# Performance work log

Measured on AMD Instinct MI355X. Metric: run time of the kernel, lower is better.

The kernel has to match this reference:

```python
import jax, jax.numpy as jnp
import numpy as np

HIDDEN = 256
HEADS = 8
HEAD_DIM = HIDDEN // HEADS
N = 4096
EPS = 1e-5


def setup_inputs() -> dict:
    key = jax.random.key(0)
    ks = jax.random.split(key, 16)
    s = HIDDEN ** -0.5
    inp = {
        "A": jax.random.uniform(ks[0], (N, N), dtype=jnp.float32),
        "h": jax.random.normal(ks[1], (N, HIDDEN), dtype=jnp.float32),
        # Linear layers stored torch-style as [out, in]
        "Wq": jax.random.normal(ks[2], (HIDDEN, HIDDEN), jnp.float32) * s,
        "bq": jnp.zeros((HIDDEN,), jnp.float32),
        "Wk": jax.random.normal(ks[3], (HIDDEN, HIDDEN), jnp.float32) * s,
        "bk": jnp.zeros((HIDDEN,), jnp.float32),
        "Wv": jax.random.normal(ks[4], (HIDDEN, HIDDEN), jnp.float32) * s,
        "bv": jnp.zeros((HIDDEN,), jnp.float32),
        "Wo": jax.random.normal(ks[5], (HIDDEN, HIDDEN), jnp.float32) * s,
        "bo": jnp.zeros((HIDDEN,), jnp.float32),
        "W1": jax.random.normal(ks[6], (2 * HIDDEN, HIDDEN), jnp.float32) * s,
        "c1": jnp.zeros((2 * HIDDEN,), jnp.float32),
        "W2": jax.random.normal(ks[7], (HIDDEN, 2 * HIDDEN), jnp.float32) * (2 * HIDDEN) ** -0.5,
        "c2": jnp.zeros((HIDDEN,), jnp.float32),
        "g1": jnp.ones((HIDDEN,), jnp.float32),
        "be1": jnp.zeros((HIDDEN,), jnp.float32),
        "g2": jnp.ones((HIDDEN,), jnp.float32),
        "be2": jnp.zeros((HIDDEN,), jnp.float32),
    }
    return inp


def _batchnorm(x, gamma, beta):
    # BatchNorm1d training mode: biased batch stats over node axis
    mean = x.mean(axis=0)
    var = ((x - mean) ** 2).mean(axis=0)
    return (x - mean) * jax.lax.rsqrt(var + EPS) * gamma + beta


def _mha(A, h, Wq, bq, Wk, bk, Wv, bv, Wo, bo):
    n = h.shape[0]
    scaling = HEAD_DIM ** -0.5
    # NOTE: raw reshape [N, H*d] -> (H, N, d), exactly as the torch code (no transpose)
    q = ((h @ Wq.T + bq).reshape(HEADS, n, HEAD_DIM)) * scaling
    k = (h @ Wk.T + bk).reshape(HEADS, n, HEAD_DIM)
    v = (h @ Wv.T + bv).reshape(HEADS, n, HEAD_DIM)
    t = jnp.einsum('hnd,hmd->hnm', q, k)          # [H, N, N]
    attn = jax.nn.softmax(t * A, axis=2)          # multiplicative adjacency mask
    out = jnp.einsum('hnm,hmd->hnd', attn, v)     # [H, N, d]
    return out.reshape(n, -1) @ Wo.T + bo         # raw reshape back, as in torch


def reference(A, h, Wq, bq, Wk, bk, Wv, bv, Wo, bo, W1, c1, W2, c2, g1, be1, g2, be2):
    h1 = h
    x = _mha(A, h, Wq, bq, Wk, bk, Wv, bv, Wo, bo)
    x = _batchnorm(x + h1, g1, be1)
    h2 = x
    x = jax.nn.relu(x @ W1.T + c1) @ W2.T + c2
    return _batchnorm(h2 + x, g2, be2)
```

## Files before the change

### kernel.cpp

```cpp
#include <hip/hip_runtime.h>

#define N_NODES 4096
#define HID 256
#define NHEADS 8
#define HDIM 32
#define EPSV 1e-5f
#define M2LOG 11.541560327111707f

typedef __bf16 bf16x8 __attribute__((ext_vector_type(8)));
typedef __bf16 bf16x4 __attribute__((ext_vector_type(4)));
typedef float f32x4 __attribute__((ext_vector_type(4)));

__device__ inline float fexp2(float x) {
    float r;
    asm("v_exp_f32 %0, %1" : "=v"(r) : "v"(x));
    return r;
}

__device__ inline uint4 pack8(float4 a, float4 b) {
    bf16x8 p;
    p[0]=(__bf16)a.x; p[1]=(__bf16)a.y; p[2]=(__bf16)a.z; p[3]=(__bf16)a.w;
    p[4]=(__bf16)b.x; p[5]=(__bf16)b.y; p[6]=(__bf16)b.z; p[7]=(__bf16)b.w;
    return __builtin_bit_cast(uint4, p);
}
__device__ inline float4 nmad4(float4 x, float4 s, float4 sh) {
    return make_float4(fmaf(x.x,s.x,sh.x), fmaf(x.y,s.y,sh.y),
                       fmaf(x.z,s.z,sh.z), fmaf(x.w,s.w,sh.w));
}
__device__ inline float bflo(unsigned u) { return __builtin_bit_cast(float, u << 16); }
__device__ inline float bfhi(unsigned u) { return __builtin_bit_cast(float, u & 0xFFFF0000u); }

__launch_bounds__(256)
__global__ void gemm_mfma(const float* __restrict__ X, const float* __restrict__ W,
                          const float* __restrict__ bias, const float* __restrict__ resid,
                          float* __restrict__ C,
                          const float* __restrict__ pSin, const float* __restrict__ pQin,
                          const float* __restrict__ gamin, const float* __restrict__ betin,
                          int norm_x, int norm_r,
                          float* __restrict__ psum, float* __restrict__ pq,
                          int M, int N, int K, float scale, int do_relu) {
    __shared__ uint4 xl[2][512];
    __shared__ uint4 wl[2][256];
    __shared__ __align__(16) float nsc[256];
    __shared__ __align__(16) float nsh[256];
    const int bm = blockIdx.x * 64, bn = blockIdx.y * 32;
    const int t = threadIdx.x;
    const int w = t >> 6, l = t & 63, g = l >> 4, nl = l & 15;
    const int srow = t >> 3, seg = t & 7;
    const int sx = (seg & 3) << 1;
    const int d0 = seg*64 + (srow ^ sx);
    const int d1 = seg*64 + ((srow + 32) ^ sx);
    const int dw = seg*32 + (srow ^ sx);
    const float* xp = X + (size_t)(bm + srow)*K + seg*8;
    const float* wp = W + (size_t)(bn + srow)*K + seg*8;
    const size_t rstep = (size_t)32*K;

    if (pSin) {
        float s = 0.f, q = 0.f;
        #pragma unroll 8
        for (int b = 0; b < 64; ++b) { s += pSin[b*HID + t]; q += pQin[b*HID + t]; }
        const float m = s * (1.f/4096.f);
        const float rstd = rsqrtf(q*(1.f/4096.f) - m*m + EPSV);
        const float sc = rstd * gamin[t];
        nsc[t] = sc;
        nsh[t] = fmaf(-m, sc, betin[t]);
        __syncthreads();
    }

    f32x4 acc[2];
    acc[0] = (f32x4){0.f,0.f,0.f,0.f};
    acc[1] = (f32x4){0.f,0.f,0.f,0.f};

    {
        float4 x0 = *(const float4*)(xp),          x1 = *(const float4*)(xp + 4);
        float4 x2 = *(const float4*)(xp + rstep),  x3 = *(const float4*)(xp + rstep + 4);
        if (norm_x) {
            float4 s0 = *(const float4*)(nsc + seg*8), s1 = *(const float4*)(nsc + seg*8 + 4);
            float4 h0 = *(const float4*)(nsh + seg*8), h1 = *(const float4*)(nsh + seg*8 + 4);
            x0 = nmad4(x0,s0,h0); x1 = nmad4(x1,s1,h1);
            x2 = nmad4(x2,s0,h0); x3 = nmad4(x3,s1,h1);
        }
        float4 w0 = *(const float4*)(wp), w1 = *(const float4*)(wp + 4);
        xl[0][d0] = pack8(x0, x1); xl[0][d1] = pack8(x2, x3);
        wl[0][dw] = pack8(w0, w1);
    }
    __syncthreads();

    for (int k0 = 0; k0 < K; k0 += 64) {
        const int cur = (k0 >> 6) & 1;
        const bool nxt = (k0 + 64) < K;
        float4 nx0, nx1, nx2, nx3, nw0, nw1;
        if (nxt) {
            const int kk = k0 + 64;
            nx0 = *(const float4*)(xp + kk);          nx1 = *(const float4*)(xp + kk + 4);
            nx2 = *(const float4*)(xp + rstep + kk);  nx3 = *(const float4*)(xp + rstep + kk + 4);
            if (norm_x) {
                float4 s0 = *(const float4*)(nsc + kk + seg*8), s1 = *(const float4*)(nsc + kk + seg*8 + 4);
                float4 h0 = *(const float4*)(nsh + kk + seg*8), h1 = *(const float4*)(nsh + kk + seg*8 + 4);
                nx0 = nmad4(nx0,s0,h0); nx1 = nmad4(nx1,s1,h1);
                nx2 = nmad4(nx2,s0,h0); nx3 = nmad4(nx3,s1,h1);
            }
            nw0 = *(const float4*)(wp + kk);  nw1 = *(const float4*)(wp + kk + 4);
        }
        __builtin_amdgcn_s_setprio(1);
        #pragma unroll
        for (int ks = 0; ks < 2; ++ks) {
            bf16x8 af = __builtin_bit_cast(bf16x8, xl[cur][(ks*4 + g)*64 + ((w*16 + nl) ^ (g << 1))]);
            #pragma unroll
            for (int nf = 0; nf < 2; ++nf) {
                bf16x8 bfr = __builtin_bit_cast(bf16x8, wl[cur][(ks*4 + g)*32 + ((nf*16 + nl) ^ (g << 1))]);
                acc[nf] = __builtin_amdgcn_mfma_f32_16x16x32_bf16(af, bfr, acc[nf], 0, 0, 0);
            }
        }
        __builtin_amdgcn_s_setprio(0);
        if (nxt) {
            xl[cur^1][d0] = pack8(nx0, nx1); xl[cur^1][d1] = pack8(nx2, nx3);
            wl[cur^1][dw] = pack8(nw0, nw1);
        }
        __syncthreads();
    }

    float colS[2] = {0.f,0.f}, colQ[2] = {0.f,0.f};
    #pragma unroll
    for (int nf = 0; nf < 2; ++nf) {
        const int col = bn + nf*16 + nl;
        const float bb = bias[col];
        float rs = 1.f, rh = 0.f;
        if (norm_r) { rs = nsc[col]; rh = nsh[col]; }
        #pragma unroll
        for (int r = 0; r < 4; ++r) {
            const int row = bm + w*16 + g*4 + r;
            float v = acc[nf][r] + bb;
            if (resid) {
                float rv = resid[(size_t)row*N + col];
                v += norm_r ? fmaf(rv, rs, rh) : rv;
            }
            v *= scale;
            if (do_relu) v = fmaxf(v, 0.f);
            C[(size_t)row*N + col] = v;
            colS[nf] += v;
            colQ[nf] = fmaf(v, v, colQ[nf]);
        }
    }
    if (psum) {
        float* cs = (float*)&xl[0][0];
        float* cq = cs + 512;
        #pragma unroll
        for (int nf = 0; nf < 2; ++nf) {
            const int idx = (w*4 + g)*32 + nf*16 + nl;
            cs[idx] = colS[nf];
            cq[idx] = colQ[nf];
        }
        __syncthreads();
        if (t < 32) {
            float s = 0.f, q = 0.f;
            #pragma unroll
            for (int i = 0; i < 16; ++i) { s += cs[i*32 + t]; q += cq[i*32 + t]; }
            psum[blockIdx.x*HID + bn + t] = s;
            pq[blockIdx.x*HID + bn + t]   = q;
        }
    }
}

__launch_bounds__(256)
__global__ void gemm_wo(const __bf16* __restrict__ Opart, const float* __restrict__ Lpart,
                        int nsplit, const float* __restrict__ W,
                        const float* __restrict__ bias, const float* __restrict__ resid,
                        float* __restrict__ C, float* __restrict__ psum, float* __restrict__ pq) {
    const int N = 256, K = 256;
    __shared__ uint4 xl[2][512];
    __shared__ uint4 wl[2][256];
    const int bm = blockIdx.x * 64, bn = blockIdx.y * 32;
    const int t = threadIdx.x;
    const int w = t >> 6, l = t & 63, g = l >> 4, nl = l & 15;
    const int srow = t >> 3, seg = t & 7;
    const int sx = (seg & 3) << 1;
    const int d0 = seg*64 + (srow ^ sx);
    const int d1 = seg*64 + ((srow + 32) ^ sx);
    const int dw = seg*32 + (srow ^ sx);
    const float* wrow = W + (size_t)(bn + srow)*K;

    auto cl = [&](int row, int kp, float4& a, float4& b) {
        const size_t flat = (size_t)row*256 + kp;
        const int hn = (int)(flat >> 5);
        float L = 0.f;
        float s0=0,s1=0,s2=0,s3=0,s4=0,s5=0,s6=0,s7=0;
        for (int z = 0; z < nsplit; ++z) {
            L += Lpart[z*32768 + hn];
            uint4 u = *(const uint4*)(Opart + (size_t)z*1048576 + flat);
            s0 += bflo(u.x); s1 += bfhi(u.x);
            s2 += bflo(u.y); s3 += bfhi(u.y);
            s4 += bflo(u.z); s5 += bfhi(u.z);
            s6 += bflo(u.w); s7 += bfhi(u.w);
        }
        const float inv = 1.f / L;
        a = make_float4(s0*inv, s1*inv, s2*inv, s3*inv);
        b = make_float4(s4*inv, s5*inv, s6*inv, s7*inv);
    };
    auto wld = [&](int kp, float4& a, float4& b) {
        const int kb = (kp & ~31) + ((kp >> 3) & 3)*4;
        a = *(const float4*)(wrow + kb);
        b = *(const float4*)(wrow + kb + 16);
    };

    f32x4 acc[2];
    acc[0] = (f32x4){0.f,0.f,0.f,0.f};
    acc[1] = (f32x4){0.f,0.f,0.f,0.f};

    {
        float4 x0, x1, x2, x3, w0, w1;
        cl(bm + srow,      seg*8, x0, x1);
        cl(bm + srow + 32, seg*8, x2, x3);
        wld(seg*8, w0, w1);
        xl[0][d0] = pack8(x0, x1); xl[0][d1] = pack8(x2, x3);
        wl[0][dw] = pack8(w0, w1);
    }
    __syncthreads();

    for (int k0 = 0; k0 < K; k0 += 64) {
        const int cur = (k0 >> 6) & 1;
        const bool nxt = (k0 + 64) < K;
        float4 nx0, nx1, nx2, nx3, nw0, nw1;
        if (nxt) {
            const int kp = k0 + 64 + seg*8;
            cl(bm + srow,      kp, nx0, nx1);
            cl(bm + srow + 32, kp, nx2, nx3);
            wld(kp, nw0, nw1);
        }
        __builtin_amdgcn_s_setprio(1);
        #pragma unroll
        for (int ks = 0; ks < 2; ++ks) {
            bf16x8 af = __builtin_bit_cast(bf16x8, xl[cur][(ks*4 + g)*64 + ((w*16 + nl) ^ (g << 1))]);
            #pragma unroll
            for (int nf = 0; nf < 2; ++nf) {
                bf16x8 bfr = __builtin_bit_cast(bf16x8, wl[cur][(ks*4 + g)*32 + ((nf*16 + nl) ^ (g << 1))]);
                acc[nf] = __builtin_amdgcn_mfma_f32_16x16x32_bf16(af, bfr, acc[nf], 0, 0, 0);
            }
        }
        __builtin_amdgcn_s_setprio(0);
        if (nxt) {
            xl[cur^1][d0] = pack8(nx0, nx1); xl[cur^1][d1] = pack8(nx2, nx3);
            wl[cur^1][dw] = pack8(nw0, nw1);
        }
        __syncthreads();
    }

    float colS[2] = {0.f,0.f}, colQ[2] = {0.f,0.f};
    #pragma unroll
    for (int nf = 0; nf < 2; ++nf) {
        const int col = bn + nf*16 + nl;
        const float bb = bias[col];
        #pragma unroll
        for (int r = 0; r < 4; ++r) {
            const int row = bm + w*16 + g*4 + r;
            float v = acc[nf][r] + bb + resid[(size_t)row*N + col];
            C[(size_t)row*N + col] = v;
            colS[nf] += v;
            colQ[nf] = fmaf(v, v, colQ[nf]);
        }
    }
    {
        float* cs = (float*)&xl[0][0];
        float* cq = cs + 512;
        #pragma unroll
        for (int nf = 0; nf < 2; ++nf) {
            const int idx = (w*4 + g)*32 + nf*16 + nl;
            cs[idx] = colS[nf];
            cq[idx] = colQ[nf];
        }
        __syncthreads();
        if (t < 32) {
            float s = 0.f, q = 0.f;
            #pragma unroll
            for (int i = 0; i < 16; ++i) { s += cs[i*32 + t]; q += cq[i*32 + t]; }
            psum[blockIdx.x*HID + bn + t] = s;
            pq[blockIdx.x*HID + bn + t]   = q;
        }
    }
}

__launch_bounds__(256)
__global__ void gemm_qkv3(const float* __restrict__ X,
                          const float* __restrict__ Wq, const float* __restrict__ Wk,
                          const float* __restrict__ Wv, const float* __restrict__ bq,
                          const float* __restrict__ bk, const float* __restrict__ bv,
                          __bf16* __restrict__ qhat, __bf16* __restrict__ khat,
                          __bf16* __restrict__ vT) {
    const int K = 256;
    __shared__ uint4 xl[2][512];
    __shared__ uint4 wql[2][256];
    __shared__ uint4 wkl[2][256];
    __shared__ uint4 wvl[2][256];
    const int bm = blockIdx.x * 64, bn = blockIdx.y * 32;
    const int t = threadIdx.x;
    const int w = t >> 6, l = t & 63, g = l >> 4, nl = l & 15;
    const int srow = t >> 3, seg = t & 7;
    const int sx = (seg & 3) << 1;
    const int d0 = seg*64 + (srow ^ sx);
    const int d1 = seg*64 + ((srow + 32) ^ sx);
    const int dw = seg*32 + (srow ^ sx);
    const float* xp  = X  + (size_t)(bm + srow)*K + seg*8;
    const float* wqp = Wq + (size_t)(bn + srow)*K + seg*8;
    const float* wkp = Wk + (size_t)(bn + srow)*K + seg*8;
    const float* wvp = Wv + (size_t)(bn + srow)*K + seg*8;
    const size_t rstep = (size_t)32*K;

    f32x4 aq[2], ak[2], av[2];
    #pragma unroll
    for (int nf = 0; nf < 2; ++nf) {
        aq[nf] = (f32x4){0.f,0.f,0.f,0.f};
        ak[nf] = (f32x4){0.f,0.f,0.f,0.f};
        av[nf] = (f32x4){0.f,0.f,0.f,0.f};
    }

    {
        float4 x0 = *(const float4*)(xp),          x1 = *(const float4*)(xp + 4);
        float4 x2 = *(const float4*)(xp + rstep),  x3 = *(const float4*)(xp + rstep + 4);
        float4 q0 = *(const float4*)(wqp), q1 = *(const float4*)(wqp + 4);
        float4 k0 = *(const float4*)(wkp), k1 = *(const float4*)(wkp + 4);
        float4 v0 = *(const float4*)(wvp), v1 = *(const float4*)(wvp + 4);
        xl[0][d0] = pack8(x0, x1); xl[0][d1] = pack8(x2, x3);
        wql[0][dw] = pack8(q0, q1);
        wkl[0][dw] = pack8(k0, k1);
        wvl[0][dw] = pack8(v0, v1);
    }
    __syncthreads();

    for (int k0 = 0; k0 < K; k0 += 64) {
        const int cur = (k0 >> 6) & 1;
        const bool nxt = (k0 + 64) < K;
        float4 nx0, nx1, nx2, nx3, nq0, nq1, nk0, nk1, nv0, nv1;
        if (nxt) {
            const int kk = k0 + 64;
            nx0 = *(const float4*)(xp + kk);          nx1 = *(const float4*)(xp + kk + 4);
            nx2 = *(const float4*)(xp + rstep + kk);  nx3 = *(const float4*)(xp + rstep + kk + 4);
            nq0 = *(const float4*)(wqp + kk);  nq1 = *(const float4*)(wqp + kk + 4);
            nk0 = *(const float4*)(wkp + kk);  nk1 = *(const float4*)(wkp + kk + 4);
            nv0 = *(const float4*)(wvp + kk);  nv1 = *(const float4*)(wvp + kk + 4);
        }
        __builtin_amdgcn_s_setprio(1);
        #pragma unroll
        for (int ks = 0; ks < 2; ++ks) {
            bf16x8 af = __builtin_bit_cast(bf16x8, xl[cur][(ks*4 + g)*64 + ((w*16 + nl) ^ (g << 1))]);
            #pragma unroll
            for (int nf = 0; nf < 2; ++nf) {
                const int wi = (ks*4 + g)*32 + ((nf*16 + nl) ^ (g << 1));
                bf16x8 bq8 = __builtin_bit_cast(bf16x8, wql[cur][wi]);
                bf16x8 bk8 = __builtin_bit_cast(bf16x8, wkl[cur][wi]);
                bf16x8 bv8 = __builtin_bit_cast(bf16x8, wvl[cur][wi]);
                aq[nf] = __builtin_amdgcn_mfma_f32_16x16x32_bf16(af, bq8, aq[nf], 0, 0, 0);
                ak[nf] = __builtin_amdgcn_mfma_f32_16x16x32_bf16(af, bk8, ak[nf], 0, 0, 0);
                av[nf] = __builtin_amdgcn_mfma_f32_16x16x32_bf16(af, bv8, av[nf], 0, 0, 0);
            }
        }
        __builtin_amdgcn_s_setprio(0);
        if (nxt) {
            xl[cur^1][d0] = pack8(nx0, nx1); xl[cur^1][d1] = pack8(nx2, nx3);
            wql[cur^1][dw] = pack8(nq0, nq1);
            wkl[cur^1][dw] = pack8(nk0, nk1);
            wvl[cur^1][dw] = pack8(nv0, nv1);
        }
        __syncthreads();
    }

    const float qscale = 0.25506595325f;
    #pragma unroll
    for (int nf = 0; nf < 2; ++nf) {
        const int col = bn + nf*16 + nl;
        const float bbq = bq[col], bbk = bk[col], bbv = bv[col];
        const int dd = col & 31;
        #pragma unroll
        for (int r = 0; r < 4; ++r) {
            const int row = bm + w*16 + g*4 + r;
            const int hh = row >> 9;
            const int nn = ((row & 511) << 3) | (col >> 5);
            qhat[((size_t)(hh*4096 + nn))*32 + dd] = (__bf16)((aq[nf][r] + bbq) * qscale);
            khat[((size_t)(hh*4096 + nn))*32 + dd] = (__bf16)(ak[nf][r] + bbk);
            vT[((size_t)(hh*32 + dd))*4096 + nn]   = (__bf16)(av[nf][r] + bbv);
        }
    }
}

__launch_bounds__(512, 2)
__global__ void attn_mfma(const __bf16* __restrict__ qh_, const __bf16* __restrict__ kh,
                          const __bf16* __restrict__ vT, const float* __restrict__ A,
                          __bf16* __restrict__ Opart, float* __restrict__ Lpart, int mlen) {
    __shared__ float A_lds[2][64][68];
    __shared__ uint4 p_lds[8][4][64];

    const int t = threadIdx.x;
    const int w = t >> 6, l = t & 63;
    const int g = l >> 4, nl = l & 15;
    const int n0 = blockIdx.x * 64;
    const int z = blockIdx.y;
    const int m_begin = z * mlen;
    const int nsteps = mlen >> 6;

    bf16x8 qf[4];
    #pragma unroll
    for (int nf = 0; nf < 4; ++nf)
        qf[nf] = *(const bf16x8*)(qh_ + ((size_t)(w*4096 + n0 + nf*16 + nl))*32 + g*8);

    f32x4 oacc[4][2];
    #pragma unroll
    for (int nf = 0; nf < 4; ++nf) {
        oacc[nf][0] = (f32x4){0.f,0.f,0.f,0.f};
        oacc[nf][1] = (f32x4){0.f,0.f,0.f,0.f};
    }
    float Li[4] = {0.f, 0.f, 0.f, 0.f};

    const int aq = t >> 3, am = (t & 7) * 8;
    const float* Abase = A + (size_t)(n0 + aq)*N_NODES + m_begin + am;
    const __bf16* kbase = kh + ((size_t)w*4096 + nl)*32 + g*8;
    const __bf16* vbase = vT + ((size_t)w*32 + nl)*4096 + g*8;

    *(float4*)&A_lds[0][aq][am]   = *(const float4*)(Abase);
    *(float4*)&A_lds[0][aq][am+4] = *(const float4*)(Abase + 4);
    __syncthreads();

    for (int s = 0; s < nsteps; ++s) {
        const int cur = s & 1;
        const int m0 = m_begin + s*64;
        const bool nxt = (s + 1) < nsteps;
        float4 a0n, a1n;
        if (nxt) {
            a0n = *(const float4*)(Abase + (s+1)*64);
            a1n = *(const float4*)(Abase + (s+1)*64 + 4);
        }
        bf16x8 kf[4], vf[4];
        #pragma unroll
        for (int tt = 0; tt < 4; ++tt)
            kf[tt] = *(const bf16x8*)(kbase + (size_t)(m0 + tt*16)*32);
        #pragma unroll
        for (int half = 0; half < 2; ++half)
            #pragma unroll
            for (int dt = 0; dt < 2; ++dt)
                vf[half*2+dt] = *(const bf16x8*)(vbase + (size_t)dt*16*4096 + m0 + half*32);
        __builtin_amdgcn_sched_barrier(0);

        #pragma unroll
        for (int half = 0; half < 2; ++half) {
            #pragma unroll
            for (int tt2 = 0; tt2 < 2; ++tt2) {
                const int tt = half*2 + tt2;
                f32x4 st[4];
                __builtin_amdgcn_s_setprio(1);
                #pragma unroll
                for (int nf = 0; nf < 4; ++nf) {
                    f32x4 zz = (f32x4){0.f,0.f,0.f,0.f};
                    st[nf] = __builtin_amdgcn_mfma_f32_16x16x32_bf16(kf[tt], qf[nf], zz, 0, 0, 0);
                }
                __builtin_amdgcn_s_setprio(0);
                #pragma unroll
                for (int nf = 0; nf < 4; ++nf) {
                    const f32x4 a4 = *(const f32x4*)&A_lds[cur][nf*16 + nl][tt*16 + g*4];
                    float p0 = fexp2(fmaf(st[nf][0], a4[0], -M2LOG));
                    float p1 = fexp2(fmaf(st[nf][1], a4[1], -M2LOG));
                    float p2 = fexp2(fmaf(st[nf][2], a4[2], -M2LOG));
                    float p3 = fexp2(fmaf(st[nf][3], a4[3], -M2LOG));
                    Li[nf] += (p0 + p1) + (p2 + p3);
                    bf16x4 pk;
                    pk[0] = (__bf16)p0; pk[1] = (__bf16)p1;
                    pk[2] = (__bf16)p2; pk[3] = (__bf16)p3;
                    const int gm = tt2*2 + (g >> 1);
                    *(bf16x4*)((char*)&p_lds[w][nf][0] + (gm*16 + (nl ^ (gm << 1)))*16 + (g & 1)*8) = pk;
                }
            }
            __builtin_amdgcn_s_setprio(1);
            #pragma unroll
            for (int nf = 0; nf < 4; ++nf) {
                bf16x8 pf = __builtin_bit_cast(bf16x8, p_lds[w][nf][g*16 + (nl ^ (g << 1))]);
                oacc[nf][0] = __builtin_amdgcn_mfma_f32_16x16x32_bf16(vf[half*2+0], pf, oacc[nf][0], 0, 0, 0);
                oacc[nf][1] = __builtin_amdgcn_mfma_f32_16x16x32_bf16(vf[half*2+1], pf, oacc[nf][1], 0, 0, 0);
            }
            __builtin_amdgcn_s_setprio(0);
        }

        if (nxt) {
            *(float4*)&A_lds[cur^1][aq][am]   = a0n;
            *(float4*)&A_lds[cur^1][aq][am+4] = a1n;
        }
        __syncthreads();
    }

    #pragma unroll
    for (int nf = 0; nf < 4; ++nf) {
        Li[nf] += __shfl_xor(Li[nf], 16);
        Li[nf] += __shfl_xor(Li[nf], 32);
        const int nq = n0 + nf*16 + nl;
        __bf16* ob = Opart + ((size_t)(z*NHEADS + w)*4096 + nq)*32;
        bf16x8 pk8;
        #pragma unroll
        for (int j = 0; j < 4; ++j) {
            pk8[j]     = (__bf16)oacc[nf][0][j];
            pk8[4 + j] = (__bf16)oacc[nf][1][j];
        }
        *(bf16x8*)(ob + g*8) = pk8;
        if (g == 0)
            Lpart[(z*NHEADS + w)*4096 + nq] = Li[nf];
    }
}

__launch_bounds__(256)
__global__ void bnorm_fin_apply(const float* __restrict__ X,
                                const float* __restrict__ pS, const float* __restrict__ pQ,
                                const float* __restrict__ gam, const float* __restrict__ bet,
                                float* __restrict__ Y) {
    __shared__ __align__(16) float sc[256];
    __shared__ __align__(16) float sh[256];
    const int t = threadIdx.x;
    {
        float s = 0.f, q = 0.f;
        #pragma unroll 8
        for (int b = 0; b < 64; ++b) { s += pS[b*HID + t]; q += pQ[b*HID + t]; }
        const float m = s * (1.f/4096.f);
        const float rstd = rsqrtf(q*(1.f/4096.f) - m*m + EPSV);
        const float scv = rstd * gam[t];
        sc[t] = scv;
        sh[t] = fmaf(-m, scv, bet[t]);
    }
    __syncthreads();
    const int base0 = (blockIdx.x * 256 + t) * 16;
    #pragma unroll
    for (int j = 0; j < 4; ++j) {
        const int base = base0 + j*4;
        const int c = base & (HID - 1);
        float4 x = *(const float4*)(X + base);
        float4 o;
        o.x = fmaf(x.x, sc[c+0], sh[c+0]);
        o.y = fmaf(x.y, sc[c+1], sh[c+1]);
        o.z = fmaf(x.z, sc[c+2], sh[c+2]);
        o.w = fmaf(x.w, sc[c+3], sh[c+3]);
        *(float4*)(Y + base) = o;
    }
}

extern "C" void kernel_launch(void* const* d_in, const int* in_sizes, int n_in,
                              void* d_out, int out_size, void* d_ws, size_t ws_size,
                              hipStream_t stream) {
    const float* A  = (const float*)d_in[0];
    const float* h  = (const float*)d_in[1];
    const float* Wq = (const float*)d_in[2];
    const float* bq = (const float*)d_in[3];
    const float* Wk = (const float*)d_in[4];
    const float* bk = (const float*)d_in[5];
    const float* Wv = (const float*)d_in[6];
    const float* bv = (const float*)d_in[7];
    const float* Wo = (const float*)d_in[8];
    const float* bo = (const float*)d_in[9];
    const float* W1 = (const float*)d_in[10];
    const float* c1 = (const float*)d_in[11];
    const float* W2 = (const float*)d_in[12];
    const float* c2 = (const float*)d_in[13];
    const float* g1 = (const float*)d_in[14];
    const float* be1= (const float*)d_in[15];
    const float* g2 = (const float*)d_in[16];
    const float* be2= (const float*)d_in[17];

    char* wsb = (char*)d_ws;
    const size_t MiB = (size_t)1 << 20;
    const int nsplit = (ws_size >= 26*MiB) ? 8 : (ws_size >= 18*MiB) ? 4 : 2;
    const int mlen = N_NODES / nsplit;

    __bf16* qhat = (__bf16*)(wsb + 0*MiB);
    __bf16* khat = (__bf16*)(wsb + 2*MiB);
    __bf16* vT   = (__bf16*)(wsb + 4*MiB);
    __bf16* Opart = (__bf16*)(wsb + 8*MiB);
    float* Lpart = (float*)(wsb + 8*MiB + (size_t)nsplit*2*MiB);
    char* statb  = wsb + 8*MiB + (size_t)nsplit*2*MiB + 1*MiB;
    float* partS1 = (float*)statb;
    float* partQ1 = partS1 + 64*HID;
    float* partS2 = partQ1 + 64*HID;
    float* partQ2 = partS2 + 64*HID;
    float* Y1 = (float*)(wsb + 4*MiB);
    float* F1 = (float*)(wsb + 8*MiB);
    float* Y2 = (float*)(wsb + 0*MiB);

    gemm_qkv3<<<dim3(64, 8), 256, 0, stream>>>(h, Wq, Wk, Wv, bq, bk, bv, qhat, khat, vT);

    attn_mfma<<<dim3(64, nsplit), 512, 0, stream>>>(qhat, khat, vT, A, Opart, Lpart, mlen);

    gemm_wo<<<dim3(64, 8), 256, 0, stream>>>(Opart, Lpart, nsplit, Wo, bo, h, Y1, partS1, partQ1);

    gemm_mfma<<<dim3(64, 16), 256, 0, stream>>>(Y1, W1, c1, nullptr, F1,
                                                partS1, partQ1, g1, be1, 1, 0,
                                                nullptr, nullptr, 4096, 512, 256, 1.f, 1);
    gemm_mfma<<<dim3(64, 8), 256, 0, stream>>>(F1, W2, c2, Y1, Y2,
                                               partS1, partQ1, g1, be1, 0, 1,
                                               partS2, partQ2, 4096, 256, 512, 1.f, 0);

    bnorm_fin_apply<<<256, 256, 0, stream>>>(Y2, partS2, partQ2, g2, be2, (float*)d_out);
}
```

Baseline: 123.4 us.

## Prefetch adjacency tiles two steps ahead and use lightweight LDS barriers

Deepens the prefetch of the adjacency tile A from one step to two, holding two register sets in rotation, so global load latency is covered by two iterations of attention work. The loop is manually unrolled by two with a macro to alternate the register buffers. __syncthreads is replaced by an explicit lgkmcnt wait plus s_barrier, so the barrier does not also wait for outstanding global loads. This raises register pressure and assumes nsteps is even, since the unrolled loop runs step s+1 without checking it.

Measured after the change: 124.5 us. About the same (+0.9%).

```diff
diff --git a/kernel.cpp b/kernel.cpp
--- a/kernel.cpp
+++ b/kernel.cpp
@@ -416,72 +416,86 @@
 
     *(float4*)&A_lds[0][aq][am]   = *(const float4*)(Abase);
     *(float4*)&A_lds[0][aq][am+4] = *(const float4*)(Abase + 4);
-    __syncthreads();
-
-    for (int s = 0; s < nsteps; ++s) {
-        const int cur = s & 1;
-        const int m0 = m_begin + s*64;
-        const bool nxt = (s + 1) < nsteps;
-        float4 a0n, a1n;
-        if (nxt) {
-            a0n = *(const float4*)(Abase + (s+1)*64);
-            a1n = *(const float4*)(Abase + (s+1)*64 + 4);
-        }
-        bf16x8 kf[4], vf[4];
-        #pragma unroll
-        for (int tt = 0; tt < 4; ++tt)
-            kf[tt] = *(const bf16x8*)(kbase + (size_t)(m0 + tt*16)*32);
-        #pragma unroll
-        for (int half = 0; half < 2; ++half)
-            #pragma unroll
-            for (int dt = 0; dt < 2; ++dt)
-                vf[half*2+dt] = *(const bf16x8*)(vbase + (size_t)dt*16*4096 + m0 + half*32);
-        __builtin_amdgcn_sched_barrier(0);
-
-        #pragma unroll
-        for (int half = 0; half < 2; ++half) {
-            #pragma unroll
-            for (int tt2 = 0; tt2 < 2; ++tt2) {
-                const int tt = half*2 + tt2;
-                f32x4 st[4];
-                __builtin_amdgcn_s_setprio(1);
-                #pragma unroll
-                for (int nf = 0; nf < 4; ++nf) {
-                    f32x4 zz = (f32x4){0.f,0.f,0.f,0.f};
-                    st[nf] = __builtin_amdgcn_mfma_f32_16x16x32_bf16(kf[tt], qf[nf], zz, 0, 0, 0);
-                }
-                __builtin_amdgcn_s_setprio(0);
-                #pragma unroll
-                for (int nf = 0; nf < 4; ++nf) {
-                    const f32x4 a4 = *(const f32x4*)&A_lds[cur][nf*16 + nl][tt*16 + g*4];
-                    float p0 = fexp2(fmaf(st[nf][0], a4[0], -M2LOG));
-                    float p1 = fexp2(fmaf(st[nf][1], a4[1], -M2LOG));
-                    float p2 = fexp2(fmaf(st[nf][2], a4[2], -M2LOG));
-                    float p3 = fexp2(fmaf(st[nf][3], a4[3], -M2LOG));
-                    Li[nf] += (p0 + p1) + (p2 + p3);
-                    bf16x4 pk;
-                    pk[0] = (__bf16)p0; pk[1] = (__bf16)p1;
-                    pk[2] = (__bf16)p2; pk[3] = (__bf16)p3;
-                    const int gm = tt2*2 + (g >> 1);
-                    *(bf16x4*)((char*)&p_lds[w][nf][0] + (gm*16 + (nl ^ (gm << 1)))*16 + (g & 1)*8) = pk;
-                }
-            }
-            __builtin_amdgcn_s_setprio(1);
-            #pragma unroll
-            for (int nf = 0; nf < 4; ++nf) {
-                bf16x8 pf = __builtin_bit_cast(bf16x8, p_lds[w][nf][g*16 + (nl ^ (g << 1))]);
-                oacc[nf][0] = __builtin_amdgcn_mfma_f32_16x16x32_bf16(vf[half*2+0], pf, oacc[nf][0], 0, 0, 0);
-                oacc[nf][1] = __builtin_amdgcn_mfma_f32_16x16x32_bf16(vf[half*2+1], pf, oacc[nf][1], 0, 0, 0);
-            }
-            __builtin_amdgcn_s_setprio(0);
-        }
-
-        if (nxt) {
-            *(float4*)&A_lds[cur^1][aq][am]   = a0n;
-            *(float4*)&A_lds[cur^1][aq][am+4] = a1n;
-        }
-        __syncthreads();
-    }
+    float4 arA0, arA1, arB0, arB1;
+    {
+        const int s1 = (1 < nsteps) ? 1 : 0;
+        arA0 = *(const float4*)(Abase + s1*64);
+        arA1 = *(const float4*)(Abase + s1*64 + 4);
+    }
+    asm volatile("s_waitcnt lgkmcnt(0)" ::: "memory");
+    __builtin_amdgcn_s_barrier();
+
+#define ATTN_STEP(S, ARU0, ARU1, ARP0, ARP1)                                          \
+    {                                                                                 \
+        const int cur = (S) & 1;                                                      \
+        const int m0 = m_begin + (S)*64;                                              \
+        const int sp = ((S) + 2 < nsteps) ? (S) + 2 : (nsteps - 1);                   \
+                  \
+        ARP0 = *(const float4*)(Abase + sp*64);                                       \
+        ARP1 = *(const float4*)(Abase + sp*64 + 4);                                   \
+                 \
+        bf16x8 kf[4], vf[4];                                                          \
+        _Pragma("unroll")                                                             \
+        for (int tt = 0; tt < 4; ++tt)                                                \
+            kf[tt] = *(const bf16x8*)(kbase + (size_t)(m0 + tt*16)*32);               \
+        _Pragma("unroll")                                                             \
+        for (int half = 0; half < 2; ++half)                                          \
+            _Pragma("unroll")                                                         \
+            for (int dt = 0; dt < 2; ++dt)                                            \
+                vf[half*2+dt] = *(const bf16x8*)(vbase + (size_t)dt*16*4096 + m0 + half*32); \
+        __builtin_amdgcn_sched_barrier(0);                                            \
+        _Pragma("unroll")                                                             \
+        for (int half = 0; half < 2; ++half) {                                        \
+            _Pragma("unroll")                                                         \
+            for (int tt2 = 0; tt2 < 2; ++tt2) {                                       \
+                const int tt = half*2 + tt2;                                          \
+                f32x4 st[4];                                                          \
+                __builtin_amdgcn_s_setprio(1);                                        \
+                _Pragma("unroll")                                                     \
+                for (int nf = 0; nf < 4; ++nf) {                                      \
+                    f32x4 zz = (f32x4){0.f,0.f,0.f,0.f};                              \
+                    st[nf] = __builtin_amdgcn_mfma_f32_16x16x32_bf16(kf[tt], qf[nf], zz, 0, 0, 0); \
+                }                                                                     \
+                __builtin_amdgcn_s_setprio(0);                                        \
+                _Pragma("unroll")                                                     \
+                for (int nf = 0; nf < 4; ++nf) {                                      \
+                    const f32x4 a4 = *(const f32x4*)&A_lds[cur][nf*16 + nl][tt*16 + g*4]; \
+                    float p0 = fexp2(fmaf(st[nf][0], a4[0], -M2LOG));                 \
+                    float p1 = fexp2(fmaf(st[nf][1], a4[1], -M2LOG));                 \
+                    float p2 = fexp2(fmaf(st[nf][2], a4[2], -M2LOG));                 \
+                    float p3 = fexp2(fmaf(st[nf][3], a4[3], -M2LOG));                 \
+                    Li[nf] += (p0 + p1) + (p2 + p3);                                  \
+                    bf16x4 pk;                                                        \
+                    pk[0] = (__bf16)p0; pk[1] = (__bf16)p1;                           \
+                    pk[2] = (__bf16)p2; pk[3] = (__bf16)p3;                           \
+                    const int gm = tt2*2 + (g >> 1);                                  \
+                    *(bf16x4*)((char*)&p_lds[w][nf][0] + (gm*16 + (nl ^ (gm << 1)))*16 + (g & 1)*8) = pk; \
+                }                                                                     \
+            }                                                                         \
+            __builtin_amdgcn_s_setprio(1);                                            \
+            _Pragma("unroll")                                                         \
+            for (int nf = 0; nf < 4; ++nf) {                                          \
+                bf16x8 pf = __builtin_bit_cast(bf16x8, p_lds[w][nf][g*16 + (nl ^ (g << 1))]); \
+                oacc[nf][0] = __builtin_amdgcn_mfma_f32_16x16x32_bf16(vf[half*2+0], pf, oacc[nf][0], 0, 0, 0); \
+                oacc[nf][1] = __builtin_amdgcn_mfma_f32_16x16x32_bf16(vf[half*2+1], pf, oacc[nf][1], 0, 0, 0); \
+            }                                                                         \
+            __builtin_amdgcn_s_setprio(0);                                            \
+        }                                                                             \
+             \
+        if ((S) + 1 < nsteps) {                                                       \
+            *(float4*)&A_lds[cur^1][aq][am]   = ARU0;                                 \
+            *(float4*)&A_lds[cur^1][aq][am+4] = ARU1;                                 \
+        }                                                                             \
+               \
+        asm volatile("s_waitcnt lgkmcnt(0)" ::: "memory");                            \
+        __builtin_amdgcn_s_barrier();                                                 \
+    }
+
+    for (int s = 0; s < nsteps; s += 2) {
+        ATTN_STEP(s,     arA0, arA1, arB0, arB1);
+        ATTN_STEP(s + 1, arB0, arB1, arA0, arA1);
+    }
+#undef ATTN_STEP
 
     #pragma unroll
     for (int nf = 0; nf < 4; ++nf) {
```
